# Optimization experiments

Hardware: AMD Instinct MI355X
Metric: run time of the kernel (lower is better)

## Reference

```python
import jax, jax.numpy as jnp
import numpy as np

DIM = 768
H = 6        # pinned by router mask construction (3 logits -> 6 head gates)
HD = DIM // H  # 128
TAU = 5.0

def setup_inputs() -> dict:
    key = jax.random.key(0)
    ks = jax.random.split(key, 10)
    w = 0.02
    return {
        "x": jax.random.normal(ks[0], (4, 2048, DIM), jnp.float32),
        "latency": jax.random.uniform(ks[1], (1,), jnp.float32),
        "qkv_w": jax.random.normal(ks[2], (3 * DIM, DIM), jnp.float32) * w,
        "qkv_b": jax.random.normal(ks[3], (3 * DIM,), jnp.float32) * w,
        "proj_w": jax.random.normal(ks[4], (DIM, DIM), jnp.float32) * w,
        "proj_b": jax.random.normal(ks[5], (DIM,), jnp.float32) * w,
        "router_w": jax.random.normal(ks[6], (3, 1), jnp.float32),
        "router_b": jax.random.normal(ks[7], (3,), jnp.float32),
        # gumbel noise g = -log(Exp(1)), matching -empty.exponential_().log()
        "g1": -jnp.log(jax.random.exponential(ks[8], (3,), jnp.float32)),
        "g2": -jnp.log(jax.random.exponential(ks[9], (3,), jnp.float32)),
    }

def reference(x, latency, qkv_w, qkv_b, proj_w, proj_b, router_w, router_b, g1, g2):
    # router: Linear(1, 3) on scalar latency -> 3 logits
    logits = router_w @ latency + router_b                      # [3]
    # gumbel-sigmoid, tau=5, hard=True with straight-through estimator
    y_soft = jax.nn.sigmoid((logits + g1 - g2) / TAU)           # [3]
    y_hard = (y_soft > 0.5).astype(y_soft.dtype)
    mask3 = y_hard - jax.lax.stop_gradient(y_soft) + y_soft     # [3]
    # first logit gates 4 heads, remaining two gate one head each -> 6 heads
    mask6 = jnp.concatenate([mask3[:1], mask3[:1], mask3[:1], mask3])  # [6]
    maskC = jnp.repeat(mask6, HD)                               # [DIM]

    B, N, C = x.shape
    qkv = jnp.einsum('bnc,oc->bno', x, qkv_w) + qkv_b           # [B,N,3*DIM]
    qkv = qkv.reshape(B, N, 3, H, HD)
    q, k, v = qkv[:, :, 0], qkv[:, :, 1], qkv[:, :, 2]          # [B,N,H,HD]

    scale = HD ** -0.5
    attn = jax.nn.softmax(jnp.einsum('bqhd,bkhd->bhqk', q * scale, k), axis=-1)
    out = jnp.einsum('bhqk,bkhd->bqhd', attn, v).reshape(B, N, C)

    out = out * maskC                                            # gate heads/channels
    return jnp.einsum('bnc,oc->bno', out, proj_w) + proj_b
```

## Files before the change

### kernel.cpp

```cpp
#include <hip/hip_runtime.h>
#include <cstdint>

#define DIM_ 768
#define H_ 6
#define HD_ 128
#define NB_ 4
#define SEQ_ 2048
#define TOK_ (NB_*SEQ_)
#define OUT3_ (3*DIM_)
#define L2E 1.4426950408889634f

typedef __bf16 bf16;
typedef __bf16 bf16x4 __attribute__((ext_vector_type(4)));
typedef __bf16 bf16x8 __attribute__((ext_vector_type(8)));
typedef float f32x4 __attribute__((ext_vector_type(4)));

__device__ __forceinline__ void gload16(const void* g, void* lds) {
  __builtin_amdgcn_global_load_lds((const __attribute__((address_space(1))) void*)g,
                                   (__attribute__((address_space(3))) void*)lds,
                                   16, 0, 0);
}

__global__ void convert_kernel(const float* __restrict__ in, bf16* __restrict__ out, int n) {
  int i = (blockIdx.x * 256 + threadIdx.x) * 4;
  if (i >= n) return;
  float4 v = *reinterpret_cast<const float4*>(in + i);
  bf16x4 o = { (bf16)v.x, (bf16)v.y, (bf16)v.z, (bf16)v.w };
  *reinterpret_cast<bf16x4*>(out + i) = o;
}

__global__ void mask_kernel(const float* __restrict__ latency,
                            const float* __restrict__ rw,
                            const float* __restrict__ rb,
                            const float* __restrict__ g1,
                            const float* __restrict__ g2,
                            float* __restrict__ mask6) {
  int i = threadIdx.x;
  if (i < 6) {
    int j = (i < 4) ? 0 : (i - 3);
    float logit = rw[j] * latency[0] + rb[j];
    float z = (logit + g1[j] - g2[j]) / 5.0f;
    float ys = 1.0f / (1.0f + expf(-z));
    float yh = ys > 0.5f ? 1.0f : 0.0f;
    mask6[i] = (yh - ys) + ys;
  }
}

__global__ __launch_bounds__(256)
void qkv_gemm(const bf16* __restrict__ A, const bf16* __restrict__ W,
              const float* __restrict__ bias,
              bf16* __restrict__ q, bf16* __restrict__ k, bf16* __restrict__ vt) {
  __shared__ bf16 As[128 * 32];
  __shared__ bf16 Bs[128 * 32];
  const int tid = threadIdx.x;
  const int l = tid & 63, w = tid >> 6;
  const int lr = l & 15, lg = l >> 4;
  const int wm = w >> 1, wn = w & 1;
  const int tm = blockIdx.y * 128;
  const int on = blockIdx.x * 128;

  f32x4 acc[4][4];
#pragma unroll
  for (int i = 0; i < 4; ++i)
#pragma unroll
    for (int j = 0; j < 4; ++j) acc[i][j] = f32x4{0.f, 0.f, 0.f, 0.f};

  for (int k0 = 0; k0 < DIM_; k0 += 32) {
    __syncthreads();
#pragma unroll
    for (int u = 0; u < 2; ++u) {
      int row = w * 32 + u * 16 + (l >> 2);
      int cb = l & 3;
      gload16(A + (size_t)(tm + row) * DIM_ + k0 + cb * 8, As + (w * 32 + u * 16) * 32);
      gload16(W + (size_t)(on + row) * DIM_ + k0 + cb * 8, Bs + (w * 32 + u * 16) * 32);
    }
    __syncthreads();
    bf16x8 af[4], bfr[4];
#pragma unroll
    for (int i = 0; i < 4; ++i)
      af[i] = *reinterpret_cast<const bf16x8*>(As + (wm * 64 + i * 16 + lr) * 32 + lg * 8);
#pragma unroll
    for (int j = 0; j < 4; ++j)
      bfr[j] = *reinterpret_cast<const bf16x8*>(Bs + (wn * 64 + j * 16 + lr) * 32 + lg * 8);
#pragma unroll
    for (int i = 0; i < 4; ++i)
#pragma unroll
      for (int j = 0; j < 4; ++j)
        acc[i][j] = __builtin_amdgcn_mfma_f32_16x16x32_bf16(af[i], bfr[j], acc[i][j], 0, 0, 0);
  }

  if (on < 2 * DIM_) {
    const int s = on / DIM_;
    const float scale = 0.08838834764831845f * L2E;
#pragma unroll
    for (int i = 0; i < 4; ++i) {
      int t = tm + wm * 64 + i * 16 + lg * 4;
#pragma unroll
      for (int j = 0; j < 4; ++j) {
        int o = on + wn * 64 + j * 16 + lr;
        int rem = o - s * DIM_;
        int hh = rem >> 7, d = rem & 127;
        float bia = bias[o];
#pragma unroll
        for (int r = 0; r < 4; ++r) {
          int tt = t + r;
          int bb = tt >> 11, n = tt & 2047;
          float val = acc[i][j][r] + bia;
          if (s == 0)
            q[((size_t)(bb * H_ + hh) * SEQ_ + n) * HD_ + d] = (bf16)(val * scale);
          else
            k[((size_t)(bb * H_ + hh) * SEQ_ + n) * HD_ + d] = (bf16)val;
        }
      }
    }
  } else {
    const int hh = (on - 2 * DIM_) >> 7;
    const int bb = tm >> 11, n0 = tm & 2047;
    bf16(*Ts)[136] = reinterpret_cast<bf16(*)[136]>(As);
    for (int wc = 0; wc < 2; ++wc) {
#pragma unroll
      for (int j = 0; j < 4; ++j) {
        __syncthreads();
        if (wn == wc) {
          float bia = bias[on + wc * 64 + j * 16 + lr];
#pragma unroll
          for (int i = 0; i < 4; ++i) {
            bf16x4 pk;
#pragma unroll
            for (int r = 0; r < 4; ++r) pk[r] = (bf16)(acc[i][j][r] + bia);
            *reinterpret_cast<bf16x4*>(&Ts[lr][wm * 64 + i * 16 + lg * 4]) = pk;
          }
        }
        __syncthreads();
        int row = tid >> 4;
        int c8 = (tid & 15) * 8;
        bf16x8 v8 = *reinterpret_cast<const bf16x8*>(&Ts[row][c8]);
        int d = wc * 64 + j * 16 + row;
        *reinterpret_cast<bf16x8*>(
            vt + ((size_t)(bb * H_ + hh) * HD_ + d) * SEQ_ + n0 + c8) = v8;
      }
    }
  }
}

__global__ __launch_bounds__(256)
void proj_gemm(const bf16* __restrict__ A, const bf16* __restrict__ W,
               const float* __restrict__ bias, float* __restrict__ out) {
  __shared__ bf16 As[128 * 32];
  __shared__ bf16 Bs[128 * 32];
  const int tid = threadIdx.x;
  const int l = tid & 63, w = tid >> 6;
  const int lr = l & 15, lg = l >> 4;
  const int wm = w >> 1, wn = w & 1;
  const int tm = blockIdx.y * 128;
  const int on = blockIdx.x * 128;

  f32x4 acc[4][4];
#pragma unroll
  for (int i = 0; i < 4; ++i)
#pragma unroll
    for (int j = 0; j < 4; ++j) acc[i][j] = f32x4{0.f, 0.f, 0.f, 0.f};

  for (int k0 = 0; k0 < DIM_; k0 += 32) {
    __syncthreads();
#pragma unroll
    for (int u = 0; u < 2; ++u) {
      int row = w * 32 + u * 16 + (l >> 2);
      int cb = l & 3;
      gload16(A + (size_t)(tm + row) * DIM_ + k0 + cb * 8, As + (w * 32 + u * 16) * 32);
      gload16(W + (size_t)(on + row) * DIM_ + k0 + cb * 8, Bs + (w * 32 + u * 16) * 32);
    }
    __syncthreads();
    bf16x8 af[4], bfr[4];
#pragma unroll
    for (int i = 0; i < 4; ++i)
      af[i] = *reinterpret_cast<const bf16x8*>(As + (wm * 64 + i * 16 + lr) * 32 + lg * 8);
#pragma unroll
    for (int j = 0; j < 4; ++j)
      bfr[j] = *reinterpret_cast<const bf16x8*>(Bs + (wn * 64 + j * 16 + lr) * 32 + lg * 8);
#pragma unroll
    for (int i = 0; i < 4; ++i)
#pragma unroll
      for (int j = 0; j < 4; ++j)
        acc[i][j] = __builtin_amdgcn_mfma_f32_16x16x32_bf16(af[i], bfr[j], acc[i][j], 0, 0, 0);
  }

#pragma unroll
  for (int i = 0; i < 4; ++i) {
#pragma unroll
    for (int j = 0; j < 4; ++j) {
      int o = on + wn * 64 + j * 16 + lr;
      float bia = bias[o];
#pragma unroll
      for (int r = 0; r < 4; ++r) {
        int t = tm + wm * 64 + i * 16 + lg * 4 + r;
        out[(size_t)t * DIM_ + o] = acc[i][j][r] + bia;
      }
    }
  }
}

__global__ __launch_bounds__(256, 2)
void attn_kernel(const bf16* __restrict__ qb, const bf16* __restrict__ kb,
                 const bf16* __restrict__ vtb, const float* __restrict__ mask6,
                 bf16* __restrict__ ab) {
  __shared__ bf16 Ks[2][64 * 128];
  __shared__ bf16 Vts[2][128 * 64];
  __shared__ bf16 Ps[4][16 * 64];

  const int tid = threadIdx.x;
  const int l = tid & 63;
  const int w = tid >> 6;
  const int lr = l & 15, lg = l >> 4;
  const int bid = blockIdx.x;
  const int bh = bid % 24;
  const int qt = bid / 24;
  const int h = bh % H_;
  const int b = bh / H_;
  const int q0 = qt * 64;

  const bf16* qg = qb + (size_t)bh * SEQ_ * HD_;
  const bf16* kg = kb + (size_t)bh * SEQ_ * HD_;
  const bf16* vg = vtb + (size_t)bh * HD_ * SEQ_;

  bf16x8 qf[4];
#pragma unroll
  for (int kc = 0; kc < 4; ++kc)
    qf[kc] = *reinterpret_cast<const bf16x8*>(
        qg + (size_t)(q0 + w * 16 + lr) * HD_ + kc * 32 + lg * 8);

  f32x4 oacc[8];
#pragma unroll
  for (int df = 0; df < 8; ++df) oacc[df] = f32x4{0.f, 0.f, 0.f, 0.f};
  float m_lane = -3.0e38f;
  float m_rows[4], lrun[4];
#pragma unroll
  for (int r = 0; r < 4; ++r) { m_rows[r] = -3.0e38f; lrun[r] = 0.f; }

  bf16 one = (bf16)1.0f;
  bf16x8 ones8 = {one, one, one, one, one, one, one, one};
  char* Pw = (char*)&Ps[w][0];

  auto STAGE = [&](int j0, int buf) {
#pragma unroll
    for (int u = 0; u < 4; ++u) {
      int rk = w * 16 + u * 4 + (l >> 4);
      int blkk = l & 15;
      gload16(kg + (size_t)(j0 + rk) * HD_ + ((blkk ^ (rk & 7)) << 3),
              &Ks[buf][(w * 16 + u * 4) * 128]);
      int rv = w * 32 + u * 8 + (l >> 3);
      int blkv = l & 7;
      gload16(vg + (size_t)rv * SEQ_ + j0 + ((blkv ^ (rv & 7)) << 3),
              &Vts[buf][(w * 32 + u * 8) * 64]);
    }
  };

  STAGE(0, 0);
  __syncthreads();
  int cur = 0;

  for (int j0 = 0; j0 < SEQ_; j0 += 64) {
    int jn = (j0 + 64 < SEQ_) ? j0 + 64 : 0;
    STAGE(jn, cur ^ 1);

    const char* Kc = (const char*)&Ks[cur][0];
    const char* Vc = (const char*)&Vts[cur][0];

    f32x4 sacc[4];
#pragma unroll
    for (int cf = 0; cf < 4; ++cf) sacc[cf] = f32x4{0.f, 0.f, 0.f, 0.f};
    __builtin_amdgcn_s_setprio(1);
#pragma unroll
    for (int cf = 0; cf < 4; ++cf) {
      int n = cf * 16 + lr;
#pragma unroll
      for (int kc = 0; kc < 4; ++kc) {
        int byteoff = n * 256 + ((kc * 64 + lg * 16) ^ ((n & 7) << 4));
        bf16x8 kf = *reinterpret_cast<const bf16x8*>(Kc + byteoff);
        sacc[cf] = __builtin_amdgcn_mfma_f32_16x16x32_bf16(kf, qf[kc], sacc[cf], 0, 0, 0);
      }
    }
    __builtin_amdgcn_s_setprio(0);

    float t = sacc[0][0];
#pragma unroll
    for (int cf = 0; cf < 4; ++cf)
#pragma unroll
      for (int r = 0; r < 4; ++r) t = fmaxf(t, sacc[cf][r]);
    t = fmaxf(t, __shfl_xor(t, 16));
    t = fmaxf(t, __shfl_xor(t, 32));
    bool need = t > m_lane + 8.0f;
    if (__ballot(need) != 0ull) {
      m_lane = fmaxf(m_lane, t);
#pragma unroll
      for (int r = 0; r < 4; ++r) {
        float tr = __shfl(t, lg * 4 + r);
        float nmr = fmaxf(m_rows[r], tr);
        float c = exp2f(m_rows[r] - nmr);
        m_rows[r] = nmr;
        lrun[r] *= c;
#pragma unroll
        for (int df = 0; df < 8; ++df) oacc[df][r] *= c;
      }
    }

#pragma unroll
    for (int cf = 0; cf < 4; ++cf) {
      bf16x4 pk;
#pragma unroll
      for (int r = 0; r < 4; ++r) pk[r] = (bf16)exp2f(sacc[cf][r] - m_lane);
      int byteoff = lr * 128 + ((((cf << 1) + (lg >> 1)) ^ (lr & 7)) << 4) + ((lg & 1) << 3);
      *reinterpret_cast<bf16x4*>(Pw + byteoff) = pk;
    }

    bf16x8 pa[2];
#pragma unroll
    for (int kc = 0; kc < 2; ++kc) {
      int byteoff = lr * 128 + ((((kc << 2) + lg) ^ (lr & 7)) << 4);
      pa[kc] = *reinterpret_cast<const bf16x8*>(Pw + byteoff);
    }

    f32x4 ssum = f32x4{0.f, 0.f, 0.f, 0.f};
    ssum = __builtin_amdgcn_mfma_f32_16x16x32_bf16(pa[0], ones8, ssum, 0, 0, 0);
    ssum = __builtin_amdgcn_mfma_f32_16x16x32_bf16(pa[1], ones8, ssum, 0, 0, 0);
#pragma unroll
    for (int r = 0; r < 4; ++r) lrun[r] += ssum[r];

    __builtin_amdgcn_s_setprio(1);
#pragma unroll
    for (int df = 0; df < 8; ++df) {
      int d = df * 16 + lr;
#pragma unroll
      for (int kc = 0; kc < 2; ++kc) {
        int byteoff = d * 128 + ((kc * 64 + lg * 16) ^ ((d & 7) << 4));
        bf16x8 vf = *reinterpret_cast<const bf16x8*>(Vc + byteoff);
        oacc[df] = __builtin_amdgcn_mfma_f32_16x16x32_bf16(pa[kc], vf, oacc[df], 0, 0, 0);
      }
    }
    __builtin_amdgcn_s_setprio(0);

    __syncthreads();
    cur ^= 1;
  }

  float hm = mask6[h];
  float inv[4];
#pragma unroll
  for (int r = 0; r < 4; ++r) inv[r] = hm / lrun[r];
#pragma unroll
  for (int df = 0; df < 8; ++df) {
    int c = h * HD_ + df * 16 + lr;
#pragma unroll
    for (int r = 0; r < 4; ++r) {
      int n = q0 + w * 16 + lg * 4 + r;
      ab[((size_t)b * SEQ_ + n) * DIM_ + c] = (bf16)(oacc[df][r] * inv[r]);
    }
  }
}

extern "C" void kernel_launch(void* const* d_in, const int* in_sizes, int n_in,
                              void* d_out, int out_size, void* d_ws, size_t ws_size,
                              hipStream_t stream) {
  const float* x        = (const float*)d_in[0];
  const float* latency  = (const float*)d_in[1];
  const float* qkv_w    = (const float*)d_in[2];
  const float* qkv_b    = (const float*)d_in[3];
  const float* proj_w   = (const float*)d_in[4];
  const float* proj_b   = (const float*)d_in[5];
  const float* router_w = (const float*)d_in[6];
  const float* router_b = (const float*)d_in[7];
  const float* g1       = (const float*)d_in[8];
  const float* g2       = (const float*)d_in[9];
  float* out = (float*)d_out;

  const size_t N_X  = (size_t)TOK_ * DIM_;
  const size_t N_WQ = (size_t)OUT3_ * DIM_;
  const size_t N_WP = (size_t)DIM_ * DIM_;
  const size_t N_P  = (size_t)NB_ * H_ * SEQ_ * HD_;

  float* maskp = (float*)d_ws;
  bf16* xb  = (bf16*)((char*)d_ws + 256);
  bf16* wqb = xb + N_X;
  bf16* wpb = wqb + N_WQ;
  bf16* qbf = wpb + N_WP;
  bf16* kbf = qbf + N_P;
  bf16* vtb = kbf + N_P;
  bf16* abf = vtb + N_P;

  size_t need = 256 + 2 * (N_X + N_WQ + N_WP + 4 * N_P);
  if (ws_size < need) return;

  convert_kernel<<<(int)(N_X / 1024), 256, 0, stream>>>(x, xb, (int)N_X);
  convert_kernel<<<(int)(N_WQ / 1024), 256, 0, stream>>>(qkv_w, wqb, (int)N_WQ);
  convert_kernel<<<(int)(N_WP / 1024), 256, 0, stream>>>(proj_w, wpb, (int)N_WP);
  mask_kernel<<<1, 64, 0, stream>>>(latency, router_w, router_b, g1, g2, maskp);

  qkv_gemm<<<dim3(OUT3_ / 128, TOK_ / 128), 256, 0, stream>>>(xb, wqb, qkv_b, qbf, kbf, vtb);
  attn_kernel<<<dim3(24 * (SEQ_ / 64)), 256, 0, stream>>>(qbf, kbf, vtb, maskp, abf);
  proj_gemm<<<dim3(DIM_ / 128, TOK_ / 128), 256, 0, stream>>>(abf, wpb, proj_b, out);
}
```

Measured before the change: 196.4 us.

## Rewrite attention with 32x32 MFMA, in-register P via permlane swap, 2-wave blocks

The attention kernel moves from 16x16x32 to 32x32x16 MFMA tiles, with each of two waves owning 32 query rows instead of four waves owning 16. The P matrix is repacked in registers with v_permlane32_swap rather than round-tripped through LDS. The row sum is accumulated in scalar registers instead of through an MFMA against a ones vector. Double buffering of K/V is removed in favour of a single buffer with sync-load-sync, which gives up load/compute overlap in exchange for lower LDS use and the chance of more resident blocks.

```diff
diff --git a/kernel.cpp b/kernel.cpp
--- a/kernel.cpp
+++ b/kernel.cpp
@@ -14,6 +14,9 @@
 typedef __bf16 bf16x4 __attribute__((ext_vector_type(4)));
 typedef __bf16 bf16x8 __attribute__((ext_vector_type(8)));
 typedef float f32x4 __attribute__((ext_vector_type(4)));
+typedef float f32x16 __attribute__((ext_vector_type(16)));
+typedef unsigned int u32;
+typedef u32 u32x4 __attribute__((ext_vector_type(4)));
 
 __device__ __forceinline__ void gload16(const void* g, void* lds) {
   __builtin_amdgcn_global_load_lds((const __attribute__((address_space(1))) void*)g,
@@ -200,160 +203,149 @@
   }
 }
 
-__global__ __launch_bounds__(256, 2)
+__global__ __launch_bounds__(128)
 void attn_kernel(const bf16* __restrict__ qb, const bf16* __restrict__ kb,
                  const bf16* __restrict__ vtb, const float* __restrict__ mask6,
                  bf16* __restrict__ ab) {
-  __shared__ bf16 Ks[2][64 * 128];
-  __shared__ bf16 Vts[2][128 * 64];
-  __shared__ bf16 Ps[4][16 * 64];
+  __shared__ bf16 Ks[64 * 128];
+  __shared__ bf16 Vts[128 * 64];
 
   const int tid = threadIdx.x;
   const int l = tid & 63;
-  const int w = tid >> 6;
-  const int lr = l & 15, lg = l >> 4;
+  const int wq = tid >> 6;
+  const int kl = l & 31;
+  const int hi = l >> 5;
   const int bid = blockIdx.x;
   const int bh = bid % 24;
   const int qt = bid / 24;
   const int h = bh % H_;
   const int b = bh / H_;
-  const int q0 = qt * 64;
+  const int q0 = qt * 64 + wq * 32;
 
   const bf16* qg = qb + (size_t)bh * SEQ_ * HD_;
   const bf16* kg = kb + (size_t)bh * SEQ_ * HD_;
   const bf16* vg = vtb + (size_t)bh * HD_ * SEQ_;
 
-  bf16x8 qf[4];
-#pragma unroll
-  for (int kc = 0; kc < 4; ++kc)
+  bf16x8 qf[8];
+#pragma unroll
+  for (int kc = 0; kc < 8; ++kc)
     qf[kc] = *reinterpret_cast<const bf16x8*>(
-        qg + (size_t)(q0 + w * 16 + lr) * HD_ + kc * 32 + lg * 8);
-
-  f32x4 oacc[8];
-#pragma unroll
-  for (int df = 0; df < 8; ++df) oacc[df] = f32x4{0.f, 0.f, 0.f, 0.f};
+        qg + (size_t)(q0 + kl) * HD_ + kc * 16 + hi * 8);
+
+  f32x16 oacc[4];
+#pragma unroll
+  for (int df = 0; df < 4; ++df)
+#pragma unroll
+    for (int r = 0; r < 16; ++r) oacc[df][r] = 0.f;
   float m_lane = -3.0e38f;
-  float m_rows[4], lrun[4];
-#pragma unroll
-  for (int r = 0; r < 4; ++r) { m_rows[r] = -3.0e38f; lrun[r] = 0.f; }
-
-  bf16 one = (bf16)1.0f;
-  bf16x8 ones8 = {one, one, one, one, one, one, one, one};
-  char* Pw = (char*)&Ps[w][0];
-
-  auto STAGE = [&](int j0, int buf) {
-#pragma unroll
-    for (int u = 0; u < 4; ++u) {
-      int rk = w * 16 + u * 4 + (l >> 4);
-      int blkk = l & 15;
-      gload16(kg + (size_t)(j0 + rk) * HD_ + ((blkk ^ (rk & 7)) << 3),
-              &Ks[buf][(w * 16 + u * 4) * 128]);
-      int rv = w * 32 + u * 8 + (l >> 3);
-      int blkv = l & 7;
-      gload16(vg + (size_t)rv * SEQ_ + j0 + ((blkv ^ (rv & 7)) << 3),
-              &Vts[buf][(w * 32 + u * 8) * 64]);
-    }
-  };
-
-  STAGE(0, 0);
-  __syncthreads();
-  int cur = 0;
+  float lsum = 0.f;
 
   for (int j0 = 0; j0 < SEQ_; j0 += 64) {
-    int jn = (j0 + 64 < SEQ_) ? j0 + 64 : 0;
-    STAGE(jn, cur ^ 1);
-
-    const char* Kc = (const char*)&Ks[cur][0];
-    const char* Vc = (const char*)&Vts[cur][0];
-
-    f32x4 sacc[4];
-#pragma unroll
-    for (int cf = 0; cf < 4; ++cf) sacc[cf] = f32x4{0.f, 0.f, 0.f, 0.f};
+    __syncthreads();
+#pragma unroll
+    for (int u = 0; u < 8; ++u) {
+      int rbase = wq * 32 + u * 4;
+      int row = rbase + (l >> 4);
+      gload16(kg + (size_t)(j0 + row) * HD_ + (((l & 15) ^ (row & 7)) << 3),
+              Ks + rbase * 128);
+      int dbase = wq * 64 + u * 8;
+      int d = dbase + (l >> 3);
+      gload16(vg + (size_t)d * SEQ_ + j0 + (((l & 7) ^ (d & 7)) << 3),
+              Vts + dbase * 64);
+    }
+    __syncthreads();
+
+    f32x16 sacc[2];
+#pragma unroll
+    for (int kf = 0; kf < 2; ++kf)
+#pragma unroll
+      for (int r = 0; r < 16; ++r) sacc[kf][r] = 0.f;
     __builtin_amdgcn_s_setprio(1);
 #pragma unroll
-    for (int cf = 0; cf < 4; ++cf) {
-      int n = cf * 16 + lr;
-#pragma unroll
-      for (int kc = 0; kc < 4; ++kc) {
-        int byteoff = n * 256 + ((kc * 64 + lg * 16) ^ ((n & 7) << 4));
-        bf16x8 kf = *reinterpret_cast<const bf16x8*>(Kc + byteoff);
-        sacc[cf] = __builtin_amdgcn_mfma_f32_16x16x32_bf16(kf, qf[kc], sacc[cf], 0, 0, 0);
-      }
-    }
+    for (int kc = 0; kc < 8; ++kc)
+#pragma unroll
+      for (int kf = 0; kf < 2; ++kf) {
+        int row = kf * 32 + kl;
+        int byteoff = row * 256 + ((((kc << 1) + hi) ^ (kl & 7)) << 4);
+        bf16x8 kfr = *reinterpret_cast<const bf16x8*>((const char*)Ks + byteoff);
+        sacc[kf] = __builtin_amdgcn_mfma_f32_32x32x16_bf16(kfr, qf[kc], sacc[kf], 0, 0, 0);
+      }
     __builtin_amdgcn_s_setprio(0);
 
     float t = sacc[0][0];
 #pragma unroll
-    for (int cf = 0; cf < 4; ++cf)
-#pragma unroll
-      for (int r = 0; r < 4; ++r) t = fmaxf(t, sacc[cf][r]);
-    t = fmaxf(t, __shfl_xor(t, 16));
+    for (int kf = 0; kf < 2; ++kf)
+#pragma unroll
+      for (int r = 0; r < 16; ++r) t = fmaxf(t, sacc[kf][r]);
     t = fmaxf(t, __shfl_xor(t, 32));
     bool need = t > m_lane + 8.0f;
     if (__ballot(need) != 0ull) {
-      m_lane = fmaxf(m_lane, t);
-#pragma unroll
-      for (int r = 0; r < 4; ++r) {
-        float tr = __shfl(t, lg * 4 + r);
-        float nmr = fmaxf(m_rows[r], tr);
-        float c = exp2f(m_rows[r] - nmr);
-        m_rows[r] = nmr;
-        lrun[r] *= c;
-#pragma unroll
-        for (int df = 0; df < 8; ++df) oacc[df][r] *= c;
-      }
-    }
-
-#pragma unroll
-    for (int cf = 0; cf < 4; ++cf) {
-      bf16x4 pk;
-#pragma unroll
-      for (int r = 0; r < 4; ++r) pk[r] = (bf16)exp2f(sacc[cf][r] - m_lane);
-      int byteoff = lr * 128 + ((((cf << 1) + (lg >> 1)) ^ (lr & 7)) << 4) + ((lg & 1) << 3);
-      *reinterpret_cast<bf16x4*>(Pw + byteoff) = pk;
-    }
-
-    bf16x8 pa[2];
-#pragma unroll
-    for (int kc = 0; kc < 2; ++kc) {
-      int byteoff = lr * 128 + ((((kc << 2) + lg) ^ (lr & 7)) << 4);
-      pa[kc] = *reinterpret_cast<const bf16x8*>(Pw + byteoff);
-    }
-
-    f32x4 ssum = f32x4{0.f, 0.f, 0.f, 0.f};
-    ssum = __builtin_amdgcn_mfma_f32_16x16x32_bf16(pa[0], ones8, ssum, 0, 0, 0);
-    ssum = __builtin_amdgcn_mfma_f32_16x16x32_bf16(pa[1], ones8, ssum, 0, 0, 0);
-#pragma unroll
-    for (int r = 0; r < 4; ++r) lrun[r] += ssum[r];
+      float nm = fmaxf(m_lane, t);
+      float c = exp2f(m_lane - nm);
+      m_lane = nm;
+      lsum *= c;
+#pragma unroll
+      for (int r = 0; r < 16; ++r) {
+        float cr = __shfl(c, (r & 3) + 8 * (r >> 2) + 4 * hi);
+#pragma unroll
+        for (int df = 0; df < 4; ++df) oacc[df][r] *= cr;
+      }
+    }
+
+    u32 pp[2][8];
+#pragma unroll
+    for (int kf = 0; kf < 2; ++kf)
+#pragma unroll
+      for (int m = 0; m < 8; ++m) {
+        float e0 = exp2f(sacc[kf][2 * m] - m_lane);
+        float e1 = exp2f(sacc[kf][2 * m + 1] - m_lane);
+        lsum += e0 + e1;
+        union { u32 u; bf16 hh2[2]; } pk;
+        pk.hh2[0] = (bf16)e0; pk.hh2[1] = (bf16)e1;
+        pp[kf][m] = pk.u;
+      }
+
+    u32x4 afv[4];
+#pragma unroll
+    for (int ks = 0; ks < 4; ++ks) {
+      int f = ks >> 1, k2 = ks & 1;
+#pragma unroll
+      for (int i = 0; i < 2; ++i) {
+        u32 a = pp[f][4 * k2 + i];
+        u32 b2 = pp[f][4 * k2 + 2 + i];
+        asm volatile("v_permlane32_swap_b32 %0, %1" : "+v"(a), "+v"(b2));
+        afv[ks][i] = a;
+        afv[ks][2 + i] = b2;
+      }
+    }
 
     __builtin_amdgcn_s_setprio(1);
 #pragma unroll
-    for (int df = 0; df < 8; ++df) {
-      int d = df * 16 + lr;
-#pragma unroll
-      for (int kc = 0; kc < 2; ++kc) {
-        int byteoff = d * 128 + ((kc * 64 + lg * 16) ^ ((d & 7) << 4));
-        bf16x8 vf = *reinterpret_cast<const bf16x8*>(Vc + byteoff);
-        oacc[df] = __builtin_amdgcn_mfma_f32_16x16x32_bf16(pa[kc], vf, oacc[df], 0, 0, 0);
+    for (int df = 0; df < 4; ++df) {
+      int d = df * 32 + kl;
+#pragma unroll
+      for (int ks = 0; ks < 4; ++ks) {
+        int byteoff = d * 128 + ((((ks << 1) + hi) ^ (kl & 7)) << 4);
+        bf16x8 vf = *reinterpret_cast<const bf16x8*>((const char*)Vts + byteoff);
+        bf16x8 pa = __builtin_bit_cast(bf16x8, afv[ks]);
+        oacc[df] = __builtin_amdgcn_mfma_f32_32x32x16_bf16(pa, vf, oacc[df], 0, 0, 0);
       }
     }
     __builtin_amdgcn_s_setprio(0);
-
-    __syncthreads();
-    cur ^= 1;
-  }
-
+  }
+
+  float lt = lsum + __shfl_xor(lsum, 32);
   float hm = mask6[h];
-  float inv[4];
-#pragma unroll
-  for (int r = 0; r < 4; ++r) inv[r] = hm / lrun[r];
-#pragma unroll
-  for (int df = 0; df < 8; ++df) {
-    int c = h * HD_ + df * 16 + lr;
-#pragma unroll
-    for (int r = 0; r < 4; ++r) {
-      int n = q0 + w * 16 + lg * 4 + r;
-      ab[((size_t)b * SEQ_ + n) * DIM_ + c] = (bf16)(oacc[df][r] * inv[r]);
+  float inv_l = hm / lt;
+#pragma unroll
+  for (int r = 0; r < 16; ++r) {
+    int qloc = (r & 3) + 8 * (r >> 2) + 4 * hi;
+    float invr = __shfl(inv_l, qloc);
+    int n = q0 + qloc;
+#pragma unroll
+    for (int df = 0; df < 4; ++df) {
+      int d = df * 32 + kl;
+      ab[((size_t)b * SEQ_ + n) * DIM_ + h * HD_ + d] = (bf16)(oacc[df][r] * invr);
     }
   }
 }
@@ -396,6 +388,6 @@
   mask_kernel<<<1, 64, 0, stream>>>(latency, router_w, router_b, g1, g2, maskp);
 
   qkv_gemm<<<dim3(OUT3_ / 128, TOK_ / 128), 256, 0, stream>>>(xb, wqb, qkv_b, qbf, kbf, vtb);
-  attn_kernel<<<dim3(24 * (SEQ_ / 64)), 256, 0, stream>>>(qbf, kbf, vtb, maskp, abf);
+  attn_kernel<<<dim3(24 * (SEQ_ / 64)), 128, 0, stream>>>(qbf, kbf, vtb, maskp, abf);
   proj_gemm<<<dim3(DIM_ / 128, TOK_ / 128), 256, 0, stream>>>(abf, wpb, proj_b, out);
 }
```

Result: slower. 225.9 us (+15.0%).
